# Kernel optimization log

Measured on AMD Instinct MI355X. Metric: run time of the kernel, lower is better.

## Reference

```python
import jax, jax.numpy as jnp
import numpy as np

N = 50000       # nodes
E = 1_600_000   # edges (before self-loops)
IN = 128        # in_channels
OUT = 32        # out_channels per head
H = 2           # heads
NEG_SLOPE = 0.2 # PyG GATConv default leaky-relu slope


def setup_inputs() -> dict:
    key = jax.random.key(0)
    k = jax.random.split(key, 6)
    x = jax.random.normal(k[0], (N, IN), jnp.float32)
    edge_index = jax.random.randint(k[1], (2, E), 0, N, dtype=jnp.int64)
    W = jax.random.normal(k[2], (IN, H * OUT), jnp.float32) / np.sqrt(IN).astype(np.float32)
    att_src = jax.random.normal(k[3], (H, OUT), jnp.float32) * 0.1
    att_dst = jax.random.normal(k[4], (H, OUT), jnp.float32) * 0.1
    bias = jax.random.normal(k[5], (H * OUT,), jnp.float32) * 0.01
    return {"x": x, "edge_index": edge_index, "W": W,
            "att_src": att_src, "att_dst": att_dst, "bias": bias}


def reference(x, edge_index, W, att_src, att_dst, bias):
    n = x.shape[0]
    h_, c = att_src.shape
    # add self-loops (PyG GATConv default add_self_loops=True)
    loops = jnp.arange(n, dtype=edge_index.dtype)
    src = jnp.concatenate([edge_index[0], loops])  # [E+N]
    dst = jnp.concatenate([edge_index[1], loops])  # [E+N]
    # linear transform -> [N, H, C]
    h = (x @ W).reshape(n, h_, c)
    # per-node attention logits per head
    a_src = jnp.einsum('nhc,hc->nh', h, att_src)  # [N, H]
    a_dst = jnp.einsum('nhc,hc->nh', h, att_dst)  # [N, H]
    # per-edge scores
    e = jax.nn.leaky_relu(a_src[src] + a_dst[dst], NEG_SLOPE)  # [E+N, H]
    # segment softmax over incoming edges of each dst node
    seg_max = jax.ops.segment_max(e, dst, num_segments=n)      # [N, H]
    ex = jnp.exp(e - seg_max[dst])
    denom = jax.ops.segment_sum(ex, dst, num_segments=n)       # [N, H]
    alpha = ex / denom[dst]                                    # [E+N, H]
    # weighted scatter-aggregate of source features
    msg = alpha[:, :, None] * h[src]                           # [E+N, H, C]
    out = jax.ops.segment_sum(msg, dst, num_segments=n)        # [N, H, C]
    return out.reshape(n, h_ * c) + bias
```

## Files before the change

### kernel.cpp

```cpp
#include <hip/hip_runtime.h>
#include <hip/hip_fp16.h>

#define N_NODES 50000
#define N_EDGES 1600000
#define IN_CH   128
#define NEG     0.2f
#define NBUK    391
#define BCAP    4608
#define CAP     80
#define CHUNK   4096
#define P_BLOCKS 391
#define PT      512

static __device__ __forceinline__ __half2 u2h2(unsigned u) {
    union { unsigned u; __half2 h; } x; x.u = u; return x.h;
}

__global__ __launch_bounds__(256) void gemm_logits(
    const float* __restrict__ x, const float* __restrict__ W,
    const float* __restrict__ att_src, const float* __restrict__ att_dst,
    unsigned int* __restrict__ hI, float* __restrict__ as_, float* __restrict__ ad_,
    int* __restrict__ gcur)
{
    if (blockIdx.x == 0) {
        for (int i = threadIdx.x; i < NBUK; i += 256) gcur[i] = 0;
    }

    __shared__ float Wl[IN_CH * 64];
    for (int i = threadIdx.x; i < IN_CH * 64; i += 256) Wl[i] = W[i];
    __syncthreads();

    int gid = blockIdx.x * 256 + threadIdx.x;
    int row = gid >> 2;
    int sub = gid & 3;
    if (row >= N_NODES) return;

    float acc[16];
#pragma unroll
    for (int c = 0; c < 16; ++c) acc[c] = 0.f;

    const float* xr = x + (size_t)row * IN_CH;
    for (int k = 0; k < IN_CH; k += 4) {
        float4 xv = *(const float4*)(xr + k);
        float xs[4] = {xv.x, xv.y, xv.z, xv.w};
#pragma unroll
        for (int kk = 0; kk < 4; ++kk) {
            const float* wr = &Wl[(k + kk) * 64 + sub * 16];
#pragma unroll
            for (int c = 0; c < 16; c += 4) {
                float4 wv = *(const float4*)(wr + c);
                acc[c]     += xs[kk] * wv.x;
                acc[c + 1] += xs[kk] * wv.y;
                acc[c + 2] += xs[kk] * wv.z;
                acc[c + 3] += xs[kk] * wv.w;
            }
        }
    }

    float part[16];
#pragma unroll
    for (int i = 0; i < 16; ++i) part[i] = __shfl_xor(acc[i], 2);

    if (sub < 2) {
        union { unsigned int u[16]; uint4 v4[4]; } pk;
#pragma unroll
        for (int i = 0; i < 16; ++i) {
            pk.u[i] = (unsigned)__half_as_ushort(__float2half_rn(acc[i])) |
                      ((unsigned)__half_as_ushort(__float2half_rn(part[i])) << 16);
        }
        uint4* hp = (uint4*)(hI + (size_t)row * 32 + sub * 16);
#pragma unroll
        for (int i = 0; i < 4; ++i) hp[i] = pk.v4[i];
    }

    float s = 0.f, d = 0.f;
#pragma unroll
    for (int c = 0; c < 16; ++c) {
        s += acc[c] * att_src[sub * 16 + c];
        d += acc[c] * att_dst[sub * 16 + c];
    }
    s += __shfl_xor(s, 1);
    d += __shfl_xor(d, 1);
    if ((sub & 1) == 0) {
        as_[row * 2 + (sub >> 1)] = s;
        ad_[row * 2 + (sub >> 1)] = d;
    }
}

__global__ __launch_bounds__(PT) void partition(
    const int* __restrict__ ei, int* __restrict__ gcur,
    unsigned int* __restrict__ barr)
{
    __shared__ int hist[NBUK];
    __shared__ int start[NBUK];
    __shared__ int gbase[NBUK];
    __shared__ int lofs[NBUK];
    __shared__ int wsum[8];
    __shared__ int woff[8];
    __shared__ unsigned int buf[CHUNK];

    int tid = threadIdx.x;
    int lane = tid & 63, wid = tid >> 6;
    int cbase = blockIdx.x * CHUNK;
    int cnt = N_EDGES - cbase;
    if (cnt > CHUNK) cnt = CHUNK;
    int n4 = cnt >> 2;

    for (int i = tid; i < NBUK; i += PT) { hist[i] = 0; lofs[i] = 0; }
    __syncthreads();

    const int4* s4 = (const int4*)ei + (cbase >> 2);
    const int4* d4 = (const int4*)(ei + N_EDGES) + (cbase >> 2);

    int4 dv[2], sv[2];
#pragma unroll
    for (int i = 0; i < 2; ++i) {
        int k = i * PT + tid;
        if (k < n4) {
            dv[i] = d4[k]; sv[i] = s4[k];
            atomicAdd(&hist[dv[i].x >> 7], 1);
            atomicAdd(&hist[dv[i].y >> 7], 1);
            atomicAdd(&hist[dv[i].z >> 7], 1);
            atomicAdd(&hist[dv[i].w >> 7], 1);
        }
    }
    __syncthreads();

    int a = (tid < NBUK) ? hist[tid] : 0;
    int orig = a;
#pragma unroll
    for (int off = 1; off < 64; off <<= 1) {
        int u = __shfl_up(a, off);
        if (lane >= off) a += u;
    }
    if (lane == 63) wsum[wid] = a;
    __syncthreads();
    if (tid == 0) {
        int r = 0;
#pragma unroll
        for (int w = 0; w < 8; ++w) { woff[w] = r; r += wsum[w]; }
    }
    __syncthreads();
    a += woff[wid];
    if (tid < NBUK) {
        start[tid] = a - orig;
        gbase[tid] = atomicAdd(&gcur[tid], orig);
    }
    __syncthreads();

#pragma unroll
    for (int i = 0; i < 2; ++i) {
        int k = i * PT + tid;
        if (k < n4) {
            int dd[4] = {dv[i].x, dv[i].y, dv[i].z, dv[i].w};
            int ss[4] = {sv[i].x, sv[i].y, sv[i].z, sv[i].w};
#pragma unroll
            for (int e = 0; e < 4; ++e) {
                int d = dd[e];
                int bkt = d >> 7;
                int loc = atomicAdd(&lofs[bkt], 1);
                buf[start[bkt] + loc] =
                    (unsigned)ss[e] | ((unsigned)(d & 127) << 16) | ((unsigned)bkt << 23);
            }
        }
    }
    __syncthreads();

    for (int i = tid; i < cnt; i += PT) {
        unsigned u = buf[i];
        int bkt = u >> 23;
        int g = gbase[bkt] + (i - start[bkt]);
        if (g < BCAP) barr[(size_t)bkt * BCAP + g] = u & 0x7FFFFFu;
    }
}

__global__ __launch_bounds__(512) void aggregate(
    const unsigned int* __restrict__ hI, const float* __restrict__ as_,
    const float* __restrict__ ad_, const int* __restrict__ gcur,
    const unsigned int* __restrict__ barr, const float* __restrict__ bias,
    float* __restrict__ out)
{
    __shared__ unsigned short lcol[32 * CAP];
    __shared__ unsigned int   lq[32 * CAP];
    __shared__ float2 advl[32];
    __shared__ float  sden[64];
    __shared__ int    hist[32];

    int b     = blockIdx.x >> 2;
    int jbase = (blockIdx.x & 3) << 5;
    int tid   = threadIdx.x;
    if (tid < 32) {
        hist[tid] = 0;
        int node = b * 128 + jbase + tid;
        advl[tid] = (node < N_NODES) ? *(const float2*)(ad_ + node * 2)
                                     : make_float2(0.f, 0.f);
    }
    if (tid < 64) sden[tid] = 0.f;
    __syncthreads();

    int cnt = gcur[b];
    if (cnt > BCAP) cnt = BCAP;
    const unsigned int* bb = barr + (size_t)b * BCAP;

    for (int i = tid; i < cnt; i += 512) {
        unsigned u = bb[i];
        int r = ((int)(u >> 16) & 127) - jbase;
        if ((unsigned)r < 32u) {
            int srci = (int)(u & 0xFFFFu);
            float2 adv = advl[r];
            float2 av  = *(const float2*)(as_ + srci * 2);
            float u0 = av.x + adv.x, u1 = av.y + adv.y;
            float f0 = (u0 > 0.f) ? u0 : NEG * u0;
            float f1 = (u1 > 0.f) ? u1 : NEG * u1;
            float q0 = __expf(f0), q1 = __expf(f1);
            int k = atomicAdd(&hist[r], 1);
            if (k < CAP) {
                atomicAdd(&sden[r * 2],     q0);
                atomicAdd(&sden[r * 2 + 1], q1);
                lcol[r * CAP + k] = (unsigned short)srci;
                lq[r * CAP + k] =
                    (unsigned)__half_as_ushort(__float2half_rn(q0)) |
                    ((unsigned)__half_as_ushort(__float2half_rn(q1)) << 16);
            }
        }
    }
    __syncthreads();

    int lane = tid & 63;
    int wave = tid >> 6;
    int c    = lane & 31;
    int hv   = lane >> 5;
    float bi0 = bias[c], bi1 = bias[32 + c];

    for (int pass = 0; pass < 2; ++pass) {
        int r = pass * 16 + (wave << 1) + hv;
        int node = b * 128 + jbase + r;
        bool valid = (node < N_NODES);

        float2 adv = advl[r];
        float2 asv = valid ? *(const float2*)(as_ + node * 2) : make_float2(0.f, 0.f);

        float t0 = asv.x + adv.x, t1 = asv.y + adv.y;
        float e0 = (t0 > 0.f) ? t0 : NEG * t0;
        float e1 = (t1 > 0.f) ? t1 : NEG * t1;
        float p0s = __expf(e0), p1s = __expf(e1);
        unsigned hs = valid ? hI[(unsigned)node * 32u + c] : 0u;
        __half2 hsh = u2h2(hs);
        float self0 = p0s * __half2float(__low2half(hsh));
        float self1 = p1s * __half2float(__high2half(hsh));

        __half2 z = __float2half2_rn(0.f);
        __half2 acA = z, acB = z, acC = z, acD = z;

        int n = valid ? min(hist[r], CAP) : 0;
        int bo = r * CAP;

        int j = 0;
        for (; j + 8 <= n; j += 8) {
            ushort4 c0 = *(const ushort4*)&lcol[bo + j];
            ushort4 c1 = *(const ushort4*)&lcol[bo + j + 4];
            uint4   q0 = *(const uint4*)&lq[bo + j];
            uint4   q1 = *(const uint4*)&lq[bo + j + 4];
            unsigned vA = hI[(unsigned)c0.x * 32u + c];
            unsigned vB = hI[(unsigned)c0.y * 32u + c];
            unsigned vC = hI[(unsigned)c0.z * 32u + c];
            unsigned vD = hI[(unsigned)c0.w * 32u + c];
            unsigned vE = hI[(unsigned)c1.x * 32u + c];
            unsigned vF = hI[(unsigned)c1.y * 32u + c];
            unsigned vG = hI[(unsigned)c1.z * 32u + c];
            unsigned vH = hI[(unsigned)c1.w * 32u + c];
            acA = __hfma2(u2h2(vA), u2h2(q0.x), acA);
            acB = __hfma2(u2h2(vB), u2h2(q0.y), acB);
            acC = __hfma2(u2h2(vC), u2h2(q0.z), acC);
            acD = __hfma2(u2h2(vD), u2h2(q0.w), acD);
            acA = __hfma2(u2h2(vE), u2h2(q1.x), acA);
            acB = __hfma2(u2h2(vF), u2h2(q1.y), acB);
            acC = __hfma2(u2h2(vG), u2h2(q1.z), acC);
            acD = __hfma2(u2h2(vH), u2h2(q1.w), acD);
        }
        for (; j < n; ++j) {
            unsigned srci = lcol[bo + j];
            unsigned qp   = lq[bo + j];
            unsigned vA = hI[srci * 32u + c];
            acA = __hfma2(u2h2(vA), u2h2(qp), acA);
        }

        float2 fA = __half22float2(acA);
        float2 fB = __half22float2(acB);
        float2 fC = __half22float2(acC);
        float2 fD = __half22float2(acD);
        float acc0 = (fA.x + fB.x) + (fC.x + fD.x) + self0;
        float acc1 = (fA.y + fB.y) + (fC.y + fD.y) + self1;

        float s0 = sden[r * 2]     + p0s;
        float s1 = sden[r * 2 + 1] + p1s;

        if (valid) {
            out[(size_t)node * 64 + c]      = acc0 / s0 + bi0;
            out[(size_t)node * 64 + 32 + c] = acc1 / s1 + bi1;
        }
    }
}

extern "C" void kernel_launch(void* const* d_in, const int* in_sizes, int n_in,
                              void* d_out, int out_size, void* d_ws, size_t ws_size,
                              hipStream_t stream)
{
    const float* x       = (const float*)d_in[0];
    const int*   ei      = (const int*)d_in[1];
    const float* W       = (const float*)d_in[2];
    const float* att_src = (const float*)d_in[3];
    const float* att_dst = (const float*)d_in[4];
    const float* bias    = (const float*)d_in[5];
    float* out = (float*)d_out;

    char* ws = (char*)d_ws;
    size_t off = 0;
    auto alloc = [&](size_t bytes) -> void* {
        void* p = ws + off;
        off = (off + bytes + 511) & ~(size_t)511;
        return p;
    };
    unsigned int* hI  = (unsigned int*)alloc((size_t)N_NODES * 32 * 4);
    float*  as_ = (float*)alloc((size_t)N_NODES * 2 * 4);
    float*  ad_ = (float*)alloc((size_t)N_NODES * 2 * 4);
    int*    gcur = (int*)alloc((size_t)NBUK * 4);
    unsigned int* barr = (unsigned int*)alloc((size_t)NBUK * BCAP * 4);

    gemm_logits<<<(N_NODES * 4 + 255) / 256, 256, 0, stream>>>(
        x, W, att_src, att_dst, hI, as_, ad_, gcur);
    partition<<<P_BLOCKS, PT, 0, stream>>>(ei, gcur, barr);
    aggregate<<<NBUK * 4, 512, 0, stream>>>(hI, as_, ad_, gcur, barr, bias, out);
}
```

Baseline: 86.92 us.

## Split aggregation into a CSR-building exp pass and a per-node gather kernel

Adds an order_exp kernel that reads each 128-node bucket once, computes per-destination degree, padded row offsets, edge exp weights and denominators, and writes a global CSR-like layout (column, fp16 weight pair). The aggregate kernel then processes nodes directly from this global layout, one half-wave per node. Previously each bucket was scanned four times (once per 32-node sub-block) and neighbor lists were capped at CAP in LDS. The cost is an extra kernel launch plus writing and re-reading about 1.6M column and weight entries through global memory.

```diff
diff --git a/kernel.cpp b/kernel.cpp
--- a/kernel.cpp
+++ b/kernel.cpp
@@ -7,7 +7,7 @@
 #define NEG     0.2f
 #define NBUK    391
 #define BCAP    4608
-#define CAP     80
+#define BCAP2   5632
 #define CHUNK   4096
 #define P_BLOCKS 391
 #define PT      512
@@ -174,132 +174,161 @@
     }
 }
 
-__global__ __launch_bounds__(512) void aggregate(
-    const unsigned int* __restrict__ hI, const float* __restrict__ as_,
-    const float* __restrict__ ad_, const int* __restrict__ gcur,
-    const unsigned int* __restrict__ barr, const float* __restrict__ bias,
-    float* __restrict__ out)
-{
-    __shared__ unsigned short lcol[32 * CAP];
-    __shared__ unsigned int   lq[32 * CAP];
-    __shared__ float2 advl[32];
-    __shared__ float  sden[64];
-    __shared__ int    hist[32];
-
-    int b     = blockIdx.x >> 2;
-    int jbase = (blockIdx.x & 3) << 5;
-    int tid   = threadIdx.x;
-    if (tid < 32) {
-        hist[tid] = 0;
-        int node = b * 128 + jbase + tid;
+__global__ __launch_bounds__(512) void order_exp(
+    const unsigned int* __restrict__ barr, const int* __restrict__ gcur,
+    const float* __restrict__ as_, const float* __restrict__ ad_,
+    unsigned short* __restrict__ gcol, unsigned int* __restrict__ gq,
+    float* __restrict__ sden, int* __restrict__ deg, int* __restrict__ rowptr)
+{
+    __shared__ int hist[128];
+    __shared__ int startb[128];
+    __shared__ int lofs[128];
+    __shared__ float lden[256];
+    __shared__ float2 advl[128];
+    __shared__ int wtot;
+
+    int b = blockIdx.x, tid = threadIdx.x;
+    if (tid < 128) {
+        hist[tid] = 0; lofs[tid] = 0;
+        int node = b * 128 + tid;
         advl[tid] = (node < N_NODES) ? *(const float2*)(ad_ + node * 2)
                                      : make_float2(0.f, 0.f);
     }
-    if (tid < 64) sden[tid] = 0.f;
+    if (tid < 256) lden[tid] = 0.f;
     __syncthreads();
 
     int cnt = gcur[b];
     if (cnt > BCAP) cnt = BCAP;
     const unsigned int* bb = barr + (size_t)b * BCAP;
 
+    for (int i = tid; i < cnt; i += 512)
+        atomicAdd(&hist[(bb[i] >> 16) & 127], 1);
+    __syncthreads();
+
+    int a = 0, orig = 0;
+    if (tid < 128) {
+        orig = (hist[tid] + 7) & ~7;
+        a = orig;
+#pragma unroll
+        for (int off = 1; off < 64; off <<= 1) {
+            int u = __shfl_up(a, off);
+            if ((tid & 63) >= off) a += u;
+        }
+    }
+    if (tid == 63) wtot = a;
+    __syncthreads();
+    if (tid >= 64 && tid < 128) a += wtot;
+    if (tid < 128) {
+        int st = a - orig;
+        startb[tid] = st;
+        int node = b * 128 + tid;
+        if (node < N_NODES) {
+            deg[node] = hist[tid];
+            rowptr[node] = b * BCAP2 + st;
+        }
+    }
+    __syncthreads();
+
     for (int i = tid; i < cnt; i += 512) {
         unsigned u = bb[i];
-        int r = ((int)(u >> 16) & 127) - jbase;
-        if ((unsigned)r < 32u) {
-            int srci = (int)(u & 0xFFFFu);
-            float2 adv = advl[r];
-            float2 av  = *(const float2*)(as_ + srci * 2);
-            float u0 = av.x + adv.x, u1 = av.y + adv.y;
-            float f0 = (u0 > 0.f) ? u0 : NEG * u0;
-            float f1 = (u1 > 0.f) ? u1 : NEG * u1;
-            float q0 = __expf(f0), q1 = __expf(f1);
-            int k = atomicAdd(&hist[r], 1);
-            if (k < CAP) {
-                atomicAdd(&sden[r * 2],     q0);
-                atomicAdd(&sden[r * 2 + 1], q1);
-                lcol[r * CAP + k] = (unsigned short)srci;
-                lq[r * CAP + k] =
-                    (unsigned)__half_as_ushort(__float2half_rn(q0)) |
-                    ((unsigned)__half_as_ushort(__float2half_rn(q1)) << 16);
-            }
-        }
-    }
-    __syncthreads();
-
-    int lane = tid & 63;
-    int wave = tid >> 6;
+        int dl = (u >> 16) & 127;
+        int srci = (int)(u & 0xFFFFu);
+        float2 adv = advl[dl];
+        float2 av  = *(const float2*)(as_ + srci * 2);
+        float u0 = av.x + adv.x, u1 = av.y + adv.y;
+        float f0 = (u0 > 0.f) ? u0 : NEG * u0;
+        float f1 = (u1 > 0.f) ? u1 : NEG * u1;
+        float q0 = __expf(f0), q1 = __expf(f1);
+        atomicAdd(&lden[dl * 2],     q0);
+        atomicAdd(&lden[dl * 2 + 1], q1);
+        int k = startb[dl] + atomicAdd(&lofs[dl], 1);
+        gcol[(size_t)b * BCAP2 + k] = (unsigned short)srci;
+        gq[(size_t)b * BCAP2 + k] =
+            (unsigned)__half_as_ushort(__float2half_rn(q0)) |
+            ((unsigned)__half_as_ushort(__float2half_rn(q1)) << 16);
+    }
+    __syncthreads();
+
+    if (tid < 256) {
+        int node = b * 128 + (tid >> 1);
+        if (node < N_NODES) sden[node * 2 + (tid & 1)] = lden[tid];
+    }
+}
+
+__global__ __launch_bounds__(256) void aggregate(
+    const unsigned int* __restrict__ hI, const float* __restrict__ as_,
+    const float* __restrict__ ad_, const int* __restrict__ deg,
+    const int* __restrict__ rowptr, const unsigned short* __restrict__ gcol,
+    const unsigned int* __restrict__ gq, const float* __restrict__ sden,
+    const float* __restrict__ bias, float* __restrict__ out)
+{
+    int lane = threadIdx.x & 63;
     int c    = lane & 31;
-    int hv   = lane >> 5;
-    float bi0 = bias[c], bi1 = bias[32 + c];
-
-    for (int pass = 0; pass < 2; ++pass) {
-        int r = pass * 16 + (wave << 1) + hv;
-        int node = b * 128 + jbase + r;
-        bool valid = (node < N_NODES);
-
-        float2 adv = advl[r];
-        float2 asv = valid ? *(const float2*)(as_ + node * 2) : make_float2(0.f, 0.f);
-
-        float t0 = asv.x + adv.x, t1 = asv.y + adv.y;
-        float e0 = (t0 > 0.f) ? t0 : NEG * t0;
-        float e1 = (t1 > 0.f) ? t1 : NEG * t1;
-        float p0s = __expf(e0), p1s = __expf(e1);
-        unsigned hs = valid ? hI[(unsigned)node * 32u + c] : 0u;
-        __half2 hsh = u2h2(hs);
-        float self0 = p0s * __half2float(__low2half(hsh));
-        float self1 = p1s * __half2float(__high2half(hsh));
-
-        __half2 z = __float2half2_rn(0.f);
-        __half2 acA = z, acB = z, acC = z, acD = z;
-
-        int n = valid ? min(hist[r], CAP) : 0;
-        int bo = r * CAP;
-
-        int j = 0;
-        for (; j + 8 <= n; j += 8) {
-            ushort4 c0 = *(const ushort4*)&lcol[bo + j];
-            ushort4 c1 = *(const ushort4*)&lcol[bo + j + 4];
-            uint4   q0 = *(const uint4*)&lq[bo + j];
-            uint4   q1 = *(const uint4*)&lq[bo + j + 4];
-            unsigned vA = hI[(unsigned)c0.x * 32u + c];
-            unsigned vB = hI[(unsigned)c0.y * 32u + c];
-            unsigned vC = hI[(unsigned)c0.z * 32u + c];
-            unsigned vD = hI[(unsigned)c0.w * 32u + c];
-            unsigned vE = hI[(unsigned)c1.x * 32u + c];
-            unsigned vF = hI[(unsigned)c1.y * 32u + c];
-            unsigned vG = hI[(unsigned)c1.z * 32u + c];
-            unsigned vH = hI[(unsigned)c1.w * 32u + c];
-            acA = __hfma2(u2h2(vA), u2h2(q0.x), acA);
-            acB = __hfma2(u2h2(vB), u2h2(q0.y), acB);
-            acC = __hfma2(u2h2(vC), u2h2(q0.z), acC);
-            acD = __hfma2(u2h2(vD), u2h2(q0.w), acD);
-            acA = __hfma2(u2h2(vE), u2h2(q1.x), acA);
-            acB = __hfma2(u2h2(vF), u2h2(q1.y), acB);
-            acC = __hfma2(u2h2(vG), u2h2(q1.z), acC);
-            acD = __hfma2(u2h2(vH), u2h2(q1.w), acD);
-        }
-        for (; j < n; ++j) {
-            unsigned srci = lcol[bo + j];
-            unsigned qp   = lq[bo + j];
-            unsigned vA = hI[srci * 32u + c];
-            acA = __hfma2(u2h2(vA), u2h2(qp), acA);
-        }
-
-        float2 fA = __half22float2(acA);
-        float2 fB = __half22float2(acB);
-        float2 fC = __half22float2(acC);
-        float2 fD = __half22float2(acD);
-        float acc0 = (fA.x + fB.x) + (fC.x + fD.x) + self0;
-        float acc1 = (fA.y + fB.y) + (fC.y + fD.y) + self1;
-
-        float s0 = sden[r * 2]     + p0s;
-        float s1 = sden[r * 2 + 1] + p1s;
-
-        if (valid) {
-            out[(size_t)node * 64 + c]      = acc0 / s0 + bi0;
-            out[(size_t)node * 64 + 32 + c] = acc1 / s1 + bi1;
-        }
-    }
+    int node = blockIdx.x * 8 + ((threadIdx.x >> 6) << 1) + (lane >> 5);
+
+    float2 adv = *(const float2*)(ad_ + node * 2);
+    float2 asv = *(const float2*)(as_ + node * 2);
+
+    float t0 = asv.x + adv.x, t1 = asv.y + adv.y;
+    float e0 = (t0 > 0.f) ? t0 : NEG * t0;
+    float e1 = (t1 > 0.f) ? t1 : NEG * t1;
+    float p0s = __expf(e0), p1s = __expf(e1);
+    unsigned hs = hI[(unsigned)node * 32u + c];
+    __half2 hsh = u2h2(hs);
+    float self0 = p0s * __half2float(__low2half(hsh));
+    float self1 = p1s * __half2float(__high2half(hsh));
+
+    float2 den = *(const float2*)(sden + node * 2);
+    float s0 = den.x + p0s;
+    float s1 = den.y + p1s;
+
+    int n  = deg[node];
+    int rp = rowptr[node];
+    const unsigned short* cb = gcol + rp;
+    const unsigned int*   qb = gq + rp;
+
+    __half2 z = __float2half2_rn(0.f);
+    __half2 acA = z, acB = z, acC = z, acD = z;
+
+    int j = 0;
+    for (; j + 8 <= n; j += 8) {
+        ushort4 c0 = *(const ushort4*)(cb + j);
+        ushort4 c1 = *(const ushort4*)(cb + j + 4);
+        uint4   q0 = *(const uint4*)(qb + j);
+        uint4   q1 = *(const uint4*)(qb + j + 4);
+        unsigned vA = hI[(unsigned)c0.x * 32u + c];
+        unsigned vB = hI[(unsigned)c0.y * 32u + c];
+        unsigned vC = hI[(unsigned)c0.z * 32u + c];
+        unsigned vD = hI[(unsigned)c0.w * 32u + c];
+        unsigned vE = hI[(unsigned)c1.x * 32u + c];
+        unsigned vF = hI[(unsigned)c1.y * 32u + c];
+        unsigned vG = hI[(unsigned)c1.z * 32u + c];
+        unsigned vH = hI[(unsigned)c1.w * 32u + c];
+        acA = __hfma2(u2h2(vA), u2h2(q0.x), acA);
+        acB = __hfma2(u2h2(vB), u2h2(q0.y), acB);
+        acC = __hfma2(u2h2(vC), u2h2(q0.z), acC);
+        acD = __hfma2(u2h2(vD), u2h2(q0.w), acD);
+        acA = __hfma2(u2h2(vE), u2h2(q1.x), acA);
+        acB = __hfma2(u2h2(vF), u2h2(q1.y), acB);
+        acC = __hfma2(u2h2(vG), u2h2(q1.z), acC);
+        acD = __hfma2(u2h2(vH), u2h2(q1.w), acD);
+    }
+    for (; j < n; ++j) {
+        unsigned srci = cb[j];
+        unsigned qp   = qb[j];
+        unsigned vA = hI[srci * 32u + c];
+        acA = __hfma2(u2h2(vA), u2h2(qp), acA);
+    }
+
+    float2 fA = __half22float2(acA);
+    float2 fB = __half22float2(acB);
+    float2 fC = __half22float2(acC);
+    float2 fD = __half22float2(acD);
+    float acc0 = (fA.x + fB.x) + (fC.x + fD.x) + self0;
+    float acc1 = (fA.y + fB.y) + (fC.y + fD.y) + self1;
+
+    out[(size_t)node * 64 + c]      = acc0 / s0 + bias[c];
+    out[(size_t)node * 64 + 32 + c] = acc1 / s1 + bias[32 + c];
 }
 
 extern "C" void kernel_launch(void* const* d_in, const int* in_sizes, int n_in,
@@ -325,10 +354,17 @@
     float*  as_ = (float*)alloc((size_t)N_NODES * 2 * 4);
     float*  ad_ = (float*)alloc((size_t)N_NODES * 2 * 4);
     int*    gcur = (int*)alloc((size_t)NBUK * 4);
-    unsigned int* barr = (unsigned int*)alloc((size_t)NBUK * BCAP * 4);
+    unsigned int*   barr = (unsigned int*)alloc((size_t)NBUK * BCAP * 4);
+    unsigned short* gcol = (unsigned short*)alloc((size_t)NBUK * BCAP2 * 2);
+    unsigned int*   gq   = (unsigned int*)alloc((size_t)NBUK * BCAP2 * 4);
+    float*  sden = (float*)alloc((size_t)N_NODES * 2 * 4);
+    int*    deg  = (int*)alloc((size_t)N_NODES * 4);
+    int*    rowptr = (int*)alloc((size_t)N_NODES * 4);
 
     gemm_logits<<<(N_NODES * 4 + 255) / 256, 256, 0, stream>>>(
         x, W, att_src, att_dst, hI, as_, ad_, gcur);
     partition<<<P_BLOCKS, PT, 0, stream>>>(ei, gcur, barr);
-    aggregate<<<NBUK * 4, 512, 0, stream>>>(hI, as_, ad_, gcur, barr, bias, out);
-}
+    order_exp<<<NBUK, 512, 0, stream>>>(barr, gcur, as_, ad_, gcol, gq, sden, deg, rowptr);
+    aggregate<<<N_NODES / 8, 256, 0, stream>>>(
+        hI, as_, ad_, deg, rowptr, gcol, gq, sden, bias, out);
+}
```

After: 104.8 us. 20.5% more time.

## Move edge score computation into partition and remap aggregate blocks per XCD

Applied to the files above, without the earlier changes.

Edge attention weights (leaky-relu plus exp, packed as fp16 pairs) are now computed once per edge in the partition kernel and written to a parallel buffer. Previously each of the four aggregate sub-blocks recomputed them for every edge in its bucket. The aggregate kernel no longer uses shared-memory float atomics for the softmax denominator; it accumulates the denominator in fp16 registers during the gather loop. Its block index is also remapped so that a bucket's four sub-blocks land on the same XCD, intended to improve L2 reuse. The cost is an extra global write and read of one word per edge and lower denominator precision from fp16 accumulation.

```diff
diff --git a/kernel.cpp b/kernel.cpp
--- a/kernel.cpp
+++ b/kernel.cpp
@@ -11,6 +11,7 @@
 #define CHUNK   4096
 #define P_BLOCKS 391
 #define PT      512
+#define A_GRID  1568
 
 static __device__ __forceinline__ __half2 u2h2(unsigned u) {
     union { unsigned u; __half2 h; } x; x.u = u; return x.h;
@@ -89,7 +90,8 @@
 
 __global__ __launch_bounds__(PT) void partition(
     const int* __restrict__ ei, int* __restrict__ gcur,
-    unsigned int* __restrict__ barr)
+    unsigned int* __restrict__ barr, unsigned int* __restrict__ barq,
+    const float* __restrict__ as_, const float* __restrict__ ad_)
 {
     __shared__ int hist[NBUK];
     __shared__ int start[NBUK];
@@ -168,59 +170,59 @@
 
     for (int i = tid; i < cnt; i += PT) {
         unsigned u = buf[i];
-        int bkt = u >> 23;
+        int bkt  = u >> 23;
+        int srci = (int)(u & 0xFFFFu);
+        int dst  = (bkt << 7) | ((int)(u >> 16) & 127);
+        float2 av = *(const float2*)(as_ + srci * 2);
+        float2 bv = *(const float2*)(ad_ + dst * 2);
+        float u0 = av.x + bv.x, u1 = av.y + bv.y;
+        float f0 = (u0 > 0.f) ? u0 : NEG * u0;
+        float f1 = (u1 > 0.f) ? u1 : NEG * u1;
+        float q0 = __expf(f0), q1 = __expf(f1);
         int g = gbase[bkt] + (i - start[bkt]);
-        if (g < BCAP) barr[(size_t)bkt * BCAP + g] = u & 0x7FFFFFu;
+        if (g < BCAP) {
+            barr[(size_t)bkt * BCAP + g] = u & 0x7FFFFFu;
+            barq[(size_t)bkt * BCAP + g] =
+                (unsigned)__half_as_ushort(__float2half_rn(q0)) |
+                ((unsigned)__half_as_ushort(__float2half_rn(q1)) << 16);
+        }
     }
 }
 
 __global__ __launch_bounds__(512) void aggregate(
     const unsigned int* __restrict__ hI, const float* __restrict__ as_,
     const float* __restrict__ ad_, const int* __restrict__ gcur,
-    const unsigned int* __restrict__ barr, const float* __restrict__ bias,
-    float* __restrict__ out)
+    const unsigned int* __restrict__ barr, const unsigned int* __restrict__ barq,
+    const float* __restrict__ bias, float* __restrict__ out)
 {
     __shared__ unsigned short lcol[32 * CAP];
     __shared__ unsigned int   lq[32 * CAP];
-    __shared__ float2 advl[32];
-    __shared__ float  sden[64];
-    __shared__ int    hist[32];
-
-    int b     = blockIdx.x >> 2;
-    int jbase = (blockIdx.x & 3) << 5;
-    int tid   = threadIdx.x;
-    if (tid < 32) {
-        hist[tid] = 0;
-        int node = b * 128 + jbase + tid;
-        advl[tid] = (node < N_NODES) ? *(const float2*)(ad_ + node * 2)
-                                     : make_float2(0.f, 0.f);
-    }
-    if (tid < 64) sden[tid] = 0.f;
+    __shared__ int hist[32];
+
+    int i_    = blockIdx.x;
+    int xcd   = i_ & 7;
+    int grp   = i_ >> 3;
+    int b     = xcd * 49 + (grp >> 2);
+    int jbase = (grp & 3) << 5;
+    if (b >= NBUK) return;
+
+    int tid = threadIdx.x;
+    if (tid < 32) hist[tid] = 0;
     __syncthreads();
 
     int cnt = gcur[b];
     if (cnt > BCAP) cnt = BCAP;
     const unsigned int* bb = barr + (size_t)b * BCAP;
+    const unsigned int* bq = barq + (size_t)b * BCAP;
 
     for (int i = tid; i < cnt; i += 512) {
         unsigned u = bb[i];
         int r = ((int)(u >> 16) & 127) - jbase;
         if ((unsigned)r < 32u) {
-            int srci = (int)(u & 0xFFFFu);
-            float2 adv = advl[r];
-            float2 av  = *(const float2*)(as_ + srci * 2);
-            float u0 = av.x + adv.x, u1 = av.y + adv.y;
-            float f0 = (u0 > 0.f) ? u0 : NEG * u0;
-            float f1 = (u1 > 0.f) ? u1 : NEG * u1;
-            float q0 = __expf(f0), q1 = __expf(f1);
             int k = atomicAdd(&hist[r], 1);
             if (k < CAP) {
-                atomicAdd(&sden[r * 2],     q0);
-                atomicAdd(&sden[r * 2 + 1], q1);
-                lcol[r * CAP + k] = (unsigned short)srci;
-                lq[r * CAP + k] =
-                    (unsigned)__half_as_ushort(__float2half_rn(q0)) |
-                    ((unsigned)__half_as_ushort(__float2half_rn(q1)) << 16);
+                lcol[r * CAP + k] = (unsigned short)(u & 0xFFFFu);
+                lq[r * CAP + k] = bq[i];
             }
         }
     }
@@ -237,7 +239,7 @@
         int node = b * 128 + jbase + r;
         bool valid = (node < N_NODES);
 
-        float2 adv = advl[r];
+        float2 adv = valid ? *(const float2*)(ad_ + node * 2) : make_float2(0.f, 0.f);
         float2 asv = valid ? *(const float2*)(as_ + node * 2) : make_float2(0.f, 0.f);
 
         float t0 = asv.x + adv.x, t1 = asv.y + adv.y;
@@ -251,16 +253,18 @@
 
         __half2 z = __float2half2_rn(0.f);
         __half2 acA = z, acB = z, acC = z, acD = z;
+        __half2 dnA = z, dnB = z, dnC = z, dnD = z;
 
         int n = valid ? min(hist[r], CAP) : 0;
-        int bo = r * CAP;
+        const unsigned short* cb = &lcol[r * CAP];
+        const unsigned int*   qb = &lq[r * CAP];
 
         int j = 0;
         for (; j + 8 <= n; j += 8) {
-            ushort4 c0 = *(const ushort4*)&lcol[bo + j];
-            ushort4 c1 = *(const ushort4*)&lcol[bo + j + 4];
-            uint4   q0 = *(const uint4*)&lq[bo + j];
-            uint4   q1 = *(const uint4*)&lq[bo + j + 4];
+            ushort4 c0 = *(const ushort4*)(cb + j);
+            ushort4 c1 = *(const ushort4*)(cb + j + 4);
+            uint4   q0 = *(const uint4*)(qb + j);
+            uint4   q1 = *(const uint4*)(qb + j + 4);
             unsigned vA = hI[(unsigned)c0.x * 32u + c];
             unsigned vB = hI[(unsigned)c0.y * 32u + c];
             unsigned vC = hI[(unsigned)c0.z * 32u + c];
@@ -277,12 +281,21 @@
             acB = __hfma2(u2h2(vF), u2h2(q1.y), acB);
             acC = __hfma2(u2h2(vG), u2h2(q1.z), acC);
             acD = __hfma2(u2h2(vH), u2h2(q1.w), acD);
+            dnA = __hadd2(dnA, u2h2(q0.x));
+            dnB = __hadd2(dnB, u2h2(q0.y));
+            dnC = __hadd2(dnC, u2h2(q0.z));
+            dnD = __hadd2(dnD, u2h2(q0.w));
+            dnA = __hadd2(dnA, u2h2(q1.x));
+            dnB = __hadd2(dnB, u2h2(q1.y));
+            dnC = __hadd2(dnC, u2h2(q1.z));
+            dnD = __hadd2(dnD, u2h2(q1.w));
         }
         for (; j < n; ++j) {
-            unsigned srci = lcol[bo + j];
-            unsigned qp   = lq[bo + j];
+            unsigned srci = cb[j];
+            unsigned qp   = qb[j];
             unsigned vA = hI[srci * 32u + c];
             acA = __hfma2(u2h2(vA), u2h2(qp), acA);
+            dnA = __hadd2(dnA, u2h2(qp));
         }
 
         float2 fA = __half22float2(acA);
@@ -292,8 +305,12 @@
         float acc0 = (fA.x + fB.x) + (fC.x + fD.x) + self0;
         float acc1 = (fA.y + fB.y) + (fC.y + fD.y) + self1;
 
-        float s0 = sden[r * 2]     + p0s;
-        float s1 = sden[r * 2 + 1] + p1s;
+        float2 dA = __half22float2(dnA);
+        float2 dB = __half22float2(dnB);
+        float2 dC = __half22float2(dnC);
+        float2 dD = __half22float2(dnD);
+        float s0 = (dA.x + dB.x) + (dC.x + dD.x) + p0s;
+        float s1 = (dA.y + dB.y) + (dC.y + dD.y) + p1s;
 
         if (valid) {
             out[(size_t)node * 64 + c]      = acc0 / s0 + bi0;
@@ -326,9 +343,11 @@
     float*  ad_ = (float*)alloc((size_t)N_NODES * 2 * 4);
     int*    gcur = (int*)alloc((size_t)NBUK * 4);
     unsigned int* barr = (unsigned int*)alloc((size_t)NBUK * BCAP * 4);
+    unsigned int* barq = (unsigned int*)alloc((size_t)NBUK * BCAP * 4);
 
     gemm_logits<<<(N_NODES * 4 + 255) / 256, 256, 0, stream>>>(
         x, W, att_src, att_dst, hI, as_, ad_, gcur);
-    partition<<<P_BLOCKS, PT, 0, stream>>>(ei, gcur, barr);
-    aggregate<<<NBUK * 4, 512, 0, stream>>>(hI, as_, ad_, gcur, barr, bias, out);
-}
+    partition<<<P_BLOCKS, PT, 0, stream>>>(ei, gcur, barr, barq, as_, ad_);
+    aggregate<<<A_GRID, 512, 0, stream>>>(
+        hI, as_, ad_, gcur, barr, barq, bias, out);
+}
```

Result: no change. 87.96 us (+1.2%).
